# Kernel tuning notes

Measured on AMD Instinct MI355X. Metric: run time of the kernel, lower is better.

The kernel has to match this reference:

```python
import jax, jax.numpy as jnp
import numpy as np

FG_THR = 0.7
BG_THR = 0.3
NUM_PER_IMAGE = 256
NUM_POS_MAX = int(NUM_PER_IMAGE * 0.5)  # positive_ratio = 0.5
BBOX_W = (1.0, 1.0, 1.0, 1.0)
BETA = 1.0 / 9.0


def _permute(t, C):
    # N x (A*C) x H x W -> N x (H*W*A) x C, matching RPNLoss.permute
    N, _, H, W = t.shape
    t = t.reshape(N, -1, C, H, W)
    t = jnp.transpose(t, (0, 3, 4, 1, 2))
    return t.reshape(N, -1, C)


def _iou(a, b):
    # a: [N,4], b: [M,4] -> [N,M] (with +1 box convention, as in source)
    x_tl = jnp.maximum(a[:, None, 0], b[None, :, 0])
    y_tl = jnp.maximum(a[:, None, 1], b[None, :, 1])
    x_rb = jnp.minimum(a[:, None, 2], b[None, :, 2])
    y_rb = jnp.minimum(a[:, None, 3], b[None, :, 3])
    inter = jnp.clip(x_rb - x_tl + 1.0, 0.0) * jnp.clip(y_rb - y_tl + 1.0, 0.0)
    area1 = (a[:, 2] - a[:, 0] + 1.0) * (a[:, 3] - a[:, 1] + 1.0)
    area2 = (b[:, 2] - b[:, 0] + 1.0) * (b[:, 3] - b[:, 1] + 1.0)
    return inter / (area1[:, None] + area2[None, :] - inter)


def _encode(anchors, targets):
    ws = anchors[:, 2] - anchors[:, 0] + 1.0
    hs = anchors[:, 3] - anchors[:, 1] + 1.0
    x_ctr = anchors[:, 0] + 0.5 * ws
    y_ctr = anchors[:, 1] + 0.5 * hs
    t_ws = targets[:, 2] - targets[:, 0] + 1.0
    t_hs = targets[:, 3] - targets[:, 1] + 1.0
    t_x = targets[:, 0] + 0.5 * t_ws
    t_y = targets[:, 1] + 0.5 * t_hs
    wx, wy, ww, wh = BBOX_W
    tx = wx * (t_x - x_ctr) / ws
    ty = wy * (t_y - y_ctr) / hs
    tw = ww * jnp.log(t_ws / ws)
    th = wh * jnp.log(t_hs / hs)
    return jnp.stack([tx, ty, tw, th], axis=1)


def _bce_logits(l, t):
    return jnp.maximum(l, 0.0) - l * t + jnp.log1p(jnp.exp(-jnp.abs(l)))


def _per_image(anchor, logit, breg, size, target, key):
    N = anchor.shape[0]
    ious = _iou(anchor, target)  # [N, M]
    vals = ious.max(axis=1)
    ori = jnp.argmax(ious, axis=1).astype(jnp.int32)
    inds = jnp.where(vals < BG_THR, -1, ori)
    inds = jnp.where((vals >= BG_THR) & (vals < FG_THR), -2, inds)
    # low-quality matches: anchors achieving the per-target max IoU keep their argmax
    col_max = ious.max(axis=0)
    restore = (ious == col_max[None, :]).any(axis=1)
    inds = jnp.where(restore, ori, inds)
    # filter_anchors: keep anchors fully inside the image (size = (h, w))
    inside = (anchor[:, 0] >= 0) & (anchor[:, 1] >= 0) & \
             (anchor[:, 2] <= size[1] - 1.0) & (anchor[:, 3] <= size[0] - 1.0)
    inds = jnp.where(inside, inds, -2)

    pos = inds >= 0
    neg = inds == -1
    # random sampling via random priorities + fixed-size top_k with validity masks
    r = jax.random.uniform(key, (N,))
    pos_vals, pos_idx = jax.lax.top_k(jnp.where(pos, r, -1.0), NUM_POS_MAX)
    valid_pos = pos_vals >= 0.0
    num_pos = valid_pos.sum()
    neg_vals, neg_idx = jax.lax.top_k(jnp.where(neg, r, -1.0), NUM_PER_IMAGE)
    valid_neg = (neg_vals >= 0.0) & (jnp.arange(NUM_PER_IMAGE) < (NUM_PER_IMAGE - num_pos))

    # classification loss terms (BCE with logits); pos target 1, neg target 0
    vp = valid_pos.astype(logit.dtype)
    vn = valid_neg.astype(logit.dtype)
    cls_sum = jnp.sum(_bce_logits(logit[pos_idx], 1.0) * vp) + \
              jnp.sum(_bce_logits(logit[neg_idx], 0.0) * vn)
    count = num_pos + valid_neg.sum()

    m = jnp.clip(inds[pos_idx], 0, None)
    offsets = _encode(anchor[pos_idx], target[m])
    diff = jnp.abs(breg[pos_idx] - offsets)
    sl1 = jnp.where(diff < BETA, 0.5 * diff * diff / BETA, diff - 0.5 * BETA)
    reg_sum = jnp.sum(sl1 * vp[:, None])
    return cls_sum, count, reg_sum


def reference(anchors, logits, bbox_regs, sizes, targets):
    B = anchors.shape[0]
    log = _permute(logits, 1)[..., 0]      # [B, H*W*A]
    breg = _permute(bbox_regs, 4)          # [B, H*W*A, 4]
    keys = jax.random.split(jax.random.key(42), B)
    cls_s, cnt, reg_s = jax.vmap(_per_image)(anchors, log, breg, sizes, targets, keys)
    total = jnp.sum(cnt).astype(anchors.dtype)
    cls_loss = jnp.sum(cls_s) / total
    reg_loss = jnp.sum(reg_s) / total
    return jnp.stack([cls_loss, reg_loss])


def setup_inputs() -> dict:
    key = jax.random.key(0)
    ks = jax.random.split(key, 10)
    B, A, H, W, M = 4, 3, 168, 256, 32
    N = H * W * A
    IMG_H, IMG_W = 800.0, 1333.0
    x1 = jax.random.uniform(ks[0], (B, N)) * 1200.0
    y1 = jax.random.uniform(ks[1], (B, N)) * 700.0
    aw = jax.random.uniform(ks[2], (B, N)) * 300.0 + 16.0
    ah = jax.random.uniform(ks[3], (B, N)) * 300.0 + 16.0
    anchors = jnp.stack([x1, y1, x1 + aw, y1 + ah], axis=-1)  # some out of image -> filtered
    tx1 = jax.random.uniform(ks[4], (B, M)) * 1000.0
    ty1 = jax.random.uniform(ks[5], (B, M)) * 500.0
    tw = jax.random.uniform(ks[6], (B, M)) * 250.0 + 30.0
    th = jax.random.uniform(ks[7], (B, M)) * 200.0 + 30.0
    targets = jnp.stack([tx1, ty1, jnp.minimum(tx1 + tw, IMG_W - 1.0),
                         jnp.minimum(ty1 + th, IMG_H - 1.0)], axis=-1)
    logits = jax.random.normal(ks[8], (B, A, H, W), dtype=jnp.float32)
    bbox_regs = jax.random.normal(ks[9], (B, 4 * A, H, W), dtype=jnp.float32) * 0.1
    sizes = jnp.tile(jnp.array([IMG_H, IMG_W], dtype=jnp.float32), (B, 1))
    return {"anchors": anchors, "logits": logits, "bbox_regs": bbox_regs,
            "sizes": sizes, "targets": targets}
```

## Files before the change

### kernel.cpp

```cpp
#include <hip/hip_runtime.h>
#include <stdint.h>

#define Bn 4
#define An 3
#define Hn 168
#define Wn 256
#define Mn 32
#define HWn (Hn*Wn)
#define Nn (HWn*An)
#define POS_CAP 8192
#define NPERIM 256
#define NPOSMAX 128
#define FG_THR 0.7f
#define BG_THR 0.3f
#define BETA (1.0f/9.0f)

#define NBLK 126
#define APT 4
#define STRIDE (NBLK * 256)
#define BUCKET_CAP 256

#define OFF_POSCNT 0
#define OFF_COUNT  16
#define OFF_CLS    17
#define OFF_REG    18
#define OFF_DONE   19
#define OFF_KEYS   24
#define OFF_PCM    32
#define OFF_WPCM   16160
#define OFF_PLIST  80672
#define OFF_BINCNT 146208
#define OFF_BINBCE 150304
#define OFF_REC    154400
#define OFF_BUCKET 1186592

__device__ __forceinline__ uint32_t rotl32(uint32_t v, int n) { return (v << n) | (v >> (32 - n)); }

__device__ __forceinline__ void tf2x32(uint32_t k0, uint32_t k1, uint32_t x0, uint32_t x1,
                                       uint32_t& o0, uint32_t& o1) {
    uint32_t k2 = k0 ^ k1 ^ 0x1BD11BDAu;
    x0 += k0; x1 += k1;
    x0 += x1; x1 = rotl32(x1, 13); x1 ^= x0;
    x0 += x1; x1 = rotl32(x1, 15); x1 ^= x0;
    x0 += x1; x1 = rotl32(x1, 26); x1 ^= x0;
    x0 += x1; x1 = rotl32(x1, 6);  x1 ^= x0;
    x0 += k1; x1 += k2 + 1u;
    x0 += x1; x1 = rotl32(x1, 17); x1 ^= x0;
    x0 += x1; x1 = rotl32(x1, 29); x1 ^= x0;
    x0 += x1; x1 = rotl32(x1, 16); x1 ^= x0;
    x0 += x1; x1 = rotl32(x1, 24); x1 ^= x0;
    x0 += k2; x1 += k0 + 2u;
    x0 += x1; x1 = rotl32(x1, 13); x1 ^= x0;
    x0 += x1; x1 = rotl32(x1, 15); x1 ^= x0;
    x0 += x1; x1 = rotl32(x1, 26); x1 ^= x0;
    x0 += x1; x1 = rotl32(x1, 6);  x1 ^= x0;
    x0 += k0; x1 += k1 + 3u;
    x0 += x1; x1 = rotl32(x1, 17); x1 ^= x0;
    x0 += x1; x1 = rotl32(x1, 29); x1 ^= x0;
    x0 += x1; x1 = rotl32(x1, 16); x1 ^= x0;
    x0 += x1; x1 = rotl32(x1, 24); x1 ^= x0;
    x0 += k1; x1 += k2 + 4u;
    x0 += x1; x1 = rotl32(x1, 13); x1 ^= x0;
    x0 += x1; x1 = rotl32(x1, 15); x1 ^= x0;
    x0 += x1; x1 = rotl32(x1, 26); x1 ^= x0;
    x0 += x1; x1 = rotl32(x1, 6);  x1 ^= x0;
    x0 += k2; x1 += k0 + 5u;
    o0 = x0; o1 = x1;
}

__device__ __forceinline__ uint32_t rng_m23(uint32_t k0, uint32_t k1, uint32_t i) {
    uint32_t o0, o1;
    tf2x32(k0, k1, 0u, i, o0, o1);
    return (o0 ^ o1) >> 9;
}

__device__ __forceinline__ float iou_one(float a0, float a1, float a2, float a3,
                                         float t0, float t1, float t2, float t3) {
    float xtl = fmaxf(a0, t0), ytl = fmaxf(a1, t1);
    float xrb = fminf(a2, t2), yrb = fminf(a3, t3);
    float iw = fmaxf(xrb - xtl + 1.0f, 0.0f);
    float ih = fmaxf(yrb - ytl + 1.0f, 0.0f);
    float inter = iw * ih;
    float area1 = (a2 - a0 + 1.0f) * (a3 - a1 + 1.0f);
    float area2 = (t2 - t0 + 1.0f) * (t3 - t1 + 1.0f);
    return inter * __builtin_amdgcn_rcpf(area1 + area2 - inter);
}

__device__ __forceinline__ bool sel_less(uint2 a, uint2 b) {
    return (a.x > b.x) || (a.x == b.x && a.y < b.y);
}

__device__ void bitonic_sort_shared(uint2* buf, int n) {
    for (int k = 2; k <= n; k <<= 1) {
        for (int j = k >> 1; j > 0; j >>= 1) {
            for (int t = (int)threadIdx.x; t < n; t += 256) {
                int ixj = t ^ j;
                if (ixj > t) {
                    uint2 x = buf[t], y = buf[ixj];
                    bool up = ((t & k) == 0);
                    bool sw = up ? sel_less(y, x) : sel_less(x, y);
                    if (sw) { buf[t] = y; buf[ixj] = x; }
                }
            }
            __syncthreads();
        }
    }
}

__global__ void __launch_bounds__(256) k1_iou(const float* __restrict__ anchors,
                                              const float* __restrict__ targets,
                                              const float* __restrict__ sizes,
                                              uint32_t* __restrict__ ws) {
    const int b = blockIdx.y, j = blockIdx.x, tid = threadIdx.x;
    const int wid = tid >> 6, lane = tid & 63;

    if (b == 0 && j == 0) {
        if (tid < 24) ws[tid] = 0u;
        for (int q = tid; q < 2 * Bn * 1024; q += 256) ws[OFF_BINCNT + q] = 0u;
        if (tid == 0) {
            for (int bb = 0; bb < Bn; ++bb) {
                uint32_t o0, o1;
                tf2x32(0u, 42u, 0u, (uint32_t)bb, o0, o1);
                ws[OFF_KEYS + 2*bb] = o0; ws[OFF_KEYS + 2*bb + 1] = o1;
            }
        }
    }

    __shared__ float part[4][Mn];
    const int base = j * 256 + tid;
    float4 av[APT];
    #pragma unroll
    for (int k = 0; k < APT; ++k)
        av[k] = ((const float4*)anchors)[b * Nn + base + k * STRIDE];

    float rowmax[APT]; int ori[APT]; uint32_t tie[APT];
    #pragma unroll
    for (int k = 0; k < APT; ++k) { rowmax[k] = -1.0f; ori[k] = 0; tie[k] = 0u; }

    float mycm = 0.0f;
    #pragma unroll 4
    for (int t = 0; t < Mn; ++t) {
        float4 tv = ((const float4*)targets)[b * Mn + t];
        float io[APT];
        float m0 = 0.0f;
        #pragma unroll
        for (int k = 0; k < APT; ++k) {
            io[k] = iou_one(av[k].x, av[k].y, av[k].z, av[k].w, tv.x, tv.y, tv.z, tv.w);
            if (io[k] > rowmax[k]) { rowmax[k] = io[k]; ori[k] = t; }
            m0 = fmaxf(m0, io[k]);
        }
        #pragma unroll
        for (int o = 32; o > 0; o >>= 1) m0 = fmaxf(m0, __shfl_xor(m0, o, 64));
        if (lane == t) mycm = m0;
        #pragma unroll
        for (int k = 0; k < APT; ++k)
            tie[k] |= (io[k] == m0) ? (1u << t) : 0u;
    }

    if (lane < Mn)
        ws[OFF_WPCM + (((size_t)b * NBLK + j) * 4 + wid) * 32 + lane] = __float_as_uint(mycm);
    if (lane < Mn) part[wid][lane] = mycm;
    __syncthreads();
    if (tid < Mn) {
        float v = fmaxf(fmaxf(part[0][tid], part[1][tid]),
                        fmaxf(part[2][tid], part[3][tid]));
        ws[OFF_PCM + ((size_t)b * NBLK + j) * Mn + tid] = __float_as_uint(v);
    }

    const float sh = sizes[b * 2 + 0], sw = sizes[b * 2 + 1];
    #pragma unroll
    for (int k = 0; k < APT; ++k) {
        bool inside = (av[k].x >= 0.0f) && (av[k].y >= 0.0f) &&
                      (av[k].z <= sw - 1.0f) && (av[k].w <= sh - 1.0f);
        uint32_t fl = (uint32_t)ori[k]
                    | (inside ? 32u : 0u)
                    | (rowmax[k] >= FG_THR ? 64u : 0u)
                    | (rowmax[k] < BG_THR ? 128u : 0u);
        ((uint2*)(ws + OFF_REC))[(size_t)b * Nn + base + k * STRIDE] =
            make_uint2(tie[k], fl);
    }
}

__global__ void __launch_bounds__(256) k2_cat(const float* __restrict__ logits,
                                              uint32_t* __restrict__ ws) {
    const int b = blockIdx.y, j = blockIdx.x, tid = threadIdx.x;
    const int wid = tid >> 6, lane = tid & 63;
    __shared__ float cmf[Mn];
    __shared__ float redf[256];

    {
        int t = tid & 31, sub = tid >> 5;
        float acc = 0.0f;
        for (int jj = sub; jj < NBLK; jj += 8)
            acc = fmaxf(acc, __uint_as_float(ws[OFF_PCM + ((size_t)b * NBLK + jj) * Mn + t]));
        redf[tid] = acc;
        __syncthreads();
        if (sub == 0) {
            #pragma unroll
            for (int q = 1; q < 8; ++q) acc = fmaxf(acc, redf[t + 32 * q]);
            cmf[t] = acc;
        }
    }
    __syncthreads();

    uint32_t eqmask;
    {
        bool eq = false;
        if (lane < Mn)
            eq = (ws[OFF_WPCM + (((size_t)b * NBLK + j) * 4 + wid) * 32 + lane]
                  == __float_as_uint(cmf[lane]));
        eqmask = (uint32_t)__ballot(eq);
    }

    const int base = j * 256 + tid;
    const uint32_t key0 = ws[OFF_KEYS + 2 * b], key1 = ws[OFF_KEYS + 2 * b + 1];
    unsigned long long lt_mask = (lane == 63) ? 0x7FFFFFFFFFFFFFFFull
                                              : ((1ull << lane) - 1ull);
    #pragma unroll
    for (int k = 0; k < APT; ++k) {
        const int i = base + k * STRIDE;
        uint2 rec = ((const uint2*)(ws + OFF_REC))[(size_t)b * Nn + i];
        bool restore = (rec.x & eqmask) != 0u;
        uint32_t fl = rec.y;
        uint32_t cat = 0;
        if (fl & 32u) {
            if (restore || (fl & 64u)) cat = 2;
            else if (fl & 128u) cat = 1;
        }
        uint32_t m = rng_m23(key0, key1, (uint32_t)i);
        unsigned long long pmask = __ballot(cat == 2u);
        if (pmask) {
            int leader = __ffsll((long long)pmask) - 1;
            uint32_t bb = 0;
            if (lane == leader) bb = atomicAdd(&ws[OFF_POSCNT + b], (uint32_t)__popcll(pmask));
            bb = __shfl(bb, leader, 64);
            if (cat == 2u) {
                uint32_t p = bb + (uint32_t)__popcll(pmask & lt_mask);
                if (p < POS_CAP)
                    ((uint2*)(ws + OFF_PLIST))[(size_t)b * POS_CAP + p] =
                        make_uint2(m, (uint32_t)i | ((fl & 31u) << 17));
            }
        }
        if (cat == 1u) {
            int bin = (int)(m >> 13);
            uint32_t slot = atomicAdd(&ws[OFF_BINCNT + (b << 10) + bin], 1u);
            if (slot < BUCKET_CAP)
                ((uint2*)(ws + OFF_BUCKET))[((((size_t)b << 10) + bin) << 8) + slot] =
                    make_uint2(m, (uint32_t)i);
            int a = i % An, hw = i / An;
            float l = logits[(b * An + a) * HWn + hw];
            atomicAdd((float*)&ws[OFF_BINBCE + (b << 10) + bin],
                      fmaxf(l, 0.0f) + log1pf(expf(-fabsf(l))));
        }
    }
}

__global__ void __launch_bounds__(256) k3_final(const float* __restrict__ anchors,
                                                const float* __restrict__ targets,
                                                const float* __restrict__ logits,
                                                const float* __restrict__ bregs,
                                                uint32_t* __restrict__ ws,
                                                float* __restrict__ out) {
    const int b = blockIdx.x, tid = threadIdx.x;
    __shared__ union { uint32_t csum[256]; uint2 buf[2048]; } sh;
    __shared__ float red[256];
    __shared__ int s_bd, s_need;
    float cls = 0.0f, reg = 0.0f;

    uint4 hc = ((const uint4*)(ws + OFF_BINCNT + (b << 10)))[tid];
    uint32_t sum = hc.x + hc.y + hc.z + hc.w;
    sh.csum[tid] = sum;
    __syncthreads();
    for (int off = 1; off < 256; off <<= 1) {
        uint32_t mine = sh.csum[tid];
        uint32_t add = (tid + off < 256) ? sh.csum[tid + off] : 0u;
        __syncthreads();
        sh.csum[tid] = mine + add;
        __syncthreads();
    }
    uint32_t pc = ws[OFF_POSCNT + b];
    int num_pos = (pc < (uint32_t)NPOSMAX) ? (int)pc : NPOSMAX;
    int k_neg = NPERIM - num_pos;
    uint32_t total = sh.csum[0];
    if ((int)total < k_neg) {
        if (tid == 0) { s_bd = -1; s_need = 0; }
    } else {
        uint32_t incl = sh.csum[tid];
        uint32_t next = (tid < 255) ? sh.csum[tid + 1] : 0u;
        if ((int)incl >= k_neg && (int)next < k_neg) {
            int cum = (int)next;
            uint32_t hv[4] = { hc.x, hc.y, hc.z, hc.w };
            int boundary = -1, needed = 0;
            #pragma unroll
            for (int q = 3; q >= 0; --q) {
                int c = (int)hv[q];
                if (cum + c >= k_neg) { boundary = 4 * tid + q; needed = k_neg - cum; break; }
                cum += c;
            }
            s_bd = boundary; s_need = needed;
        }
    }
    if (tid == 0) {
        int sel_negs = ((int)total < k_neg) ? (int)total : k_neg;
        atomicAdd(&ws[OFF_COUNT], (uint32_t)(num_pos + sel_negs));
    }
    __syncthreads();
    const int bd = s_bd, need = s_need;

    {
        float4 hb = ((const float4*)(ws + OFF_BINBCE + (b << 10)))[tid];
        int bin0 = 4 * tid;
        if (bin0 + 0 > bd) cls += hb.x;
        if (bin0 + 1 > bd) cls += hb.y;
        if (bin0 + 2 > bd) cls += hb.z;
        if (bin0 + 3 > bd) cls += hb.w;
    }
    __syncthreads();

    if (need > 0) {
        int cnt = (int)ws[OFF_BINCNT + (b << 10) + bd];
        if (cnt > BUCKET_CAP) cnt = BUCKET_CAP;
        const uint2* bkt = (const uint2*)(ws + OFF_BUCKET) + ((((size_t)b << 10) + bd) << 8);
        for (int t = tid; t < cnt; t += 256) sh.buf[t] = bkt[t];
        int npad = 1; while (npad < cnt) npad <<= 1;
        for (int t = tid; t < npad; t += 256) if (t >= cnt) sh.buf[t] = make_uint2(0u, 0xFFFFFFFFu);
        __syncthreads();
        bitonic_sort_shared(sh.buf, npad);
        int sel = (need < cnt) ? need : cnt;
        for (int t = tid; t < sel; t += 256) {
            int i = (int)sh.buf[t].y;
            int a = i % An, hw = i / An;
            float l = logits[(b * An + a) * HWn + hw];
            cls += fmaxf(l, 0.0f) + log1pf(expf(-fabsf(l)));
        }
    }
    __syncthreads();

    {
        int pci = (pc < (uint32_t)POS_CAP) ? (int)pc : POS_CAP;
        const uint2* plist = (const uint2*)(ws + OFF_PLIST) + (size_t)b * POS_CAP;
        int psel = (pci < NPOSMAX) ? pci : NPOSMAX;
        bool use_buf = false;
        if (pci > NPOSMAX) {
            int n = (pci < 2048) ? pci : 2048;
            for (int t = tid; t < n; t += 256) sh.buf[t] = plist[t];
            int npad = 1; while (npad < n) npad <<= 1;
            for (int t = tid; t < npad; t += 256) if (t >= n) sh.buf[t] = make_uint2(0u, 0xFFFFFFFFu);
            __syncthreads();
            bitonic_sort_shared(sh.buf, npad);
            use_buf = true;
            psel = (NPOSMAX < n) ? NPOSMAX : n;
        }
        for (int t = tid; t < psel; t += 256) {
            uint32_t packed = use_buf ? sh.buf[t].y : plist[t].y;
            int i = (int)(packed & 0x1FFFFu);
            int orit = (int)(packed >> 17);
            int a = i % An, hw = i / An;
            float l = logits[(b * An + a) * HWn + hw];
            cls += fmaxf(l, 0.0f) - l + log1pf(expf(-fabsf(l)));
            float4 avx = ((const float4*)anchors)[b * Nn + i];
            float4 tv = ((const float4*)targets)[b * Mn + orit];
            float aws = avx.z - avx.x + 1.0f, ahs = avx.w - avx.y + 1.0f;
            float axc = avx.x + 0.5f * aws, ayc = avx.y + 0.5f * ahs;
            float tws = tv.z - tv.x + 1.0f, ths = tv.w - tv.y + 1.0f;
            float txc = tv.x + 0.5f * tws, tyc = tv.y + 0.5f * ths;
            float off0 = (txc - axc) / aws;
            float off1 = (tyc - ayc) / ahs;
            float off2 = logf(tws / aws);
            float off3 = logf(ths / ahs);
            float br0 = bregs[(b * 12 + a * 4 + 0) * HWn + hw];
            float br1 = bregs[(b * 12 + a * 4 + 1) * HWn + hw];
            float br2 = bregs[(b * 12 + a * 4 + 2) * HWn + hw];
            float br3 = bregs[(b * 12 + a * 4 + 3) * HWn + hw];
            float d;
            d = fabsf(br0 - off0); reg += (d < BETA) ? 0.5f * d * d / BETA : d - 0.5f * BETA;
            d = fabsf(br1 - off1); reg += (d < BETA) ? 0.5f * d * d / BETA : d - 0.5f * BETA;
            d = fabsf(br2 - off2); reg += (d < BETA) ? 0.5f * d * d / BETA : d - 0.5f * BETA;
            d = fabsf(br3 - off3); reg += (d < BETA) ? 0.5f * d * d / BETA : d - 0.5f * BETA;
        }
    }

    red[tid] = cls;
    __syncthreads();
    for (int s = 128; s > 0; s >>= 1) {
        if (tid < s) red[tid] += red[tid + s];
        __syncthreads();
    }
    if (tid == 0 && red[0] != 0.0f) atomicAdd((float*)&ws[OFF_CLS], red[0]);
    __syncthreads();
    red[tid] = reg;
    __syncthreads();
    for (int s = 128; s > 0; s >>= 1) {
        if (tid < s) red[tid] += red[tid + s];
        __syncthreads();
    }
    if (tid == 0) {
        if (red[0] != 0.0f) atomicAdd((float*)&ws[OFF_REG], red[0]);
        __threadfence();
        uint32_t old = atomicAdd(&ws[OFF_DONE], 1u);
        if (old == Bn - 1) {
            float cls_tot = __uint_as_float(atomicAdd(&ws[OFF_CLS], 0u));
            float reg_tot = __uint_as_float(atomicAdd(&ws[OFF_REG], 0u));
            float cnt = (float)atomicAdd(&ws[OFF_COUNT], 0u);
            out[0] = cls_tot / cnt;
            out[1] = reg_tot / cnt;
        }
    }
}

extern "C" void kernel_launch(void* const* d_in, const int* in_sizes, int n_in,
                              void* d_out, int out_size, void* d_ws, size_t ws_size,
                              hipStream_t stream) {
    const float* anchors = (const float*)d_in[0];
    const float* logits  = (const float*)d_in[1];
    const float* bregs   = (const float*)d_in[2];
    const float* sizes   = (const float*)d_in[3];
    const float* targets = (const float*)d_in[4];
    float* out = (float*)d_out;
    uint32_t* ws = (uint32_t*)d_ws;

    k1_iou<<<dim3(NBLK, Bn), dim3(256), 0, stream>>>(anchors, targets, sizes, ws);
    k2_cat<<<dim3(NBLK, Bn), dim3(256), 0, stream>>>(logits, ws);
    k3_final<<<dim3(Bn), dim3(256), 0, stream>>>(anchors, targets, logits, bregs, ws, out);
}
```

Before: 158.1 us.

## Fuse categorization into IoU kernel and defer tie-restore anchors to final kernel

Removes the separate k2_cat pass and its per-anchor record buffer. k1 now classifies anchors directly: clear positives and negatives are emitted at once, and only anchors with a tie bit that might be restored go to a compacted list. k3 computes the per-target column max, builds per-wave equality masks and resolves that deferred list. Workspace zeroing moves into a small init kernel. This saves a full read and write of per-anchor records and a launch, but puts more serial work, atomics and a possibly long tie list into the 4-block final kernel.

```diff
diff --git a/kernel.cpp b/kernel.cpp
--- a/kernel.cpp
+++ b/kernel.cpp
@@ -9,6 +9,7 @@
 #define HWn (Hn*Wn)
 #define Nn (HWn*An)
 #define POS_CAP 8192
+#define TIE_CAP 49152
 #define NPERIM 256
 #define NPOSMAX 128
 #define FG_THR 0.7f
@@ -18,21 +19,22 @@
 #define NBLK 126
 #define APT 4
 #define STRIDE (NBLK * 256)
+#define NWAVES (NBLK * 4)
 #define BUCKET_CAP 256
 
 #define OFF_POSCNT 0
-#define OFF_COUNT  16
-#define OFF_CLS    17
-#define OFF_REG    18
-#define OFF_DONE   19
-#define OFF_KEYS   24
-#define OFF_PCM    32
-#define OFF_WPCM   16160
-#define OFF_PLIST  80672
-#define OFF_BINCNT 146208
-#define OFF_BINBCE 150304
-#define OFF_REC    154400
-#define OFF_BUCKET 1186592
+#define OFF_TIECNT 4
+#define OFF_COUNT  8
+#define OFF_CLS    9
+#define OFF_REG    10
+#define OFF_DONE   11
+#define OFF_BINCNT 16
+#define OFF_BINBCE 4112
+#define ZERO_WORDS 8208
+#define OFF_WPCM   8208
+#define OFF_PLIST  72720
+#define OFF_BUCKET 138256
+#define OFF_TIE    2235408
 
 __device__ __forceinline__ uint32_t rotl32(uint32_t v, int n) { return (v << n) | (v >> (32 - n)); }
 
@@ -74,6 +76,10 @@
     return (o0 ^ o1) >> 9;
 }
 
+__device__ __forceinline__ uint32_t vload(const uint32_t* p) {
+    return *(const volatile uint32_t*)p;
+}
+
 __device__ __forceinline__ float iou_one(float a0, float a1, float a2, float a3,
                                          float t0, float t1, float t2, float t3) {
     float xtl = fmaxf(a0, t0), ytl = fmaxf(a1, t1);
@@ -84,6 +90,10 @@
     float area1 = (a2 - a0 + 1.0f) * (a3 - a1 + 1.0f);
     float area2 = (t2 - t0 + 1.0f) * (t3 - t1 + 1.0f);
     return inter * __builtin_amdgcn_rcpf(area1 + area2 - inter);
+}
+
+__device__ __forceinline__ float bce0(float l) {
+    return fmaxf(l, 0.0f) + log1pf(expf(-fabsf(l)));
 }
 
 __device__ __forceinline__ bool sel_less(uint2 a, uint2 b) {
@@ -107,26 +117,22 @@
     }
 }
 
+__global__ void __launch_bounds__(256) k0_init(uint32_t* __restrict__ ws) {
+    int i = blockIdx.x * 256 + (int)threadIdx.x;
+    if (i < ZERO_WORDS) ws[i] = 0u;
+}
+
 __global__ void __launch_bounds__(256) k1_iou(const float* __restrict__ anchors,
                                               const float* __restrict__ targets,
                                               const float* __restrict__ sizes,
+                                              const float* __restrict__ logits,
                                               uint32_t* __restrict__ ws) {
     const int b = blockIdx.y, j = blockIdx.x, tid = threadIdx.x;
     const int wid = tid >> 6, lane = tid & 63;
 
-    if (b == 0 && j == 0) {
-        if (tid < 24) ws[tid] = 0u;
-        for (int q = tid; q < 2 * Bn * 1024; q += 256) ws[OFF_BINCNT + q] = 0u;
-        if (tid == 0) {
-            for (int bb = 0; bb < Bn; ++bb) {
-                uint32_t o0, o1;
-                tf2x32(0u, 42u, 0u, (uint32_t)bb, o0, o1);
-                ws[OFF_KEYS + 2*bb] = o0; ws[OFF_KEYS + 2*bb + 1] = o1;
-            }
-        }
-    }
-
-    __shared__ float part[4][Mn];
+    uint32_t key0, key1;
+    tf2x32(0u, 42u, 0u, (uint32_t)b, key0, key1);
+
     const int base = j * 256 + tid;
     float4 av[APT];
     #pragma unroll
@@ -158,90 +164,52 @@
     }
 
     if (lane < Mn)
-        ws[OFF_WPCM + (((size_t)b * NBLK + j) * 4 + wid) * 32 + lane] = __float_as_uint(mycm);
-    if (lane < Mn) part[wid][lane] = mycm;
-    __syncthreads();
-    if (tid < Mn) {
-        float v = fmaxf(fmaxf(part[0][tid], part[1][tid]),
-                        fmaxf(part[2][tid], part[3][tid]));
-        ws[OFF_PCM + ((size_t)b * NBLK + j) * Mn + tid] = __float_as_uint(v);
-    }
+        ws[OFF_WPCM + ((size_t)b * NWAVES + (j * 4 + wid)) * 32 + lane] = __float_as_uint(mycm);
 
     const float sh = sizes[b * 2 + 0], sw = sizes[b * 2 + 1];
-    #pragma unroll
-    for (int k = 0; k < APT; ++k) {
-        bool inside = (av[k].x >= 0.0f) && (av[k].y >= 0.0f) &&
-                      (av[k].z <= sw - 1.0f) && (av[k].w <= sh - 1.0f);
-        uint32_t fl = (uint32_t)ori[k]
-                    | (inside ? 32u : 0u)
-                    | (rowmax[k] >= FG_THR ? 64u : 0u)
-                    | (rowmax[k] < BG_THR ? 128u : 0u);
-        ((uint2*)(ws + OFF_REC))[(size_t)b * Nn + base + k * STRIDE] =
-            make_uint2(tie[k], fl);
-    }
-}
-
-__global__ void __launch_bounds__(256) k2_cat(const float* __restrict__ logits,
-                                              uint32_t* __restrict__ ws) {
-    const int b = blockIdx.y, j = blockIdx.x, tid = threadIdx.x;
-    const int wid = tid >> 6, lane = tid & 63;
-    __shared__ float cmf[Mn];
-    __shared__ float redf[256];
-
-    {
-        int t = tid & 31, sub = tid >> 5;
-        float acc = 0.0f;
-        for (int jj = sub; jj < NBLK; jj += 8)
-            acc = fmaxf(acc, __uint_as_float(ws[OFF_PCM + ((size_t)b * NBLK + jj) * Mn + t]));
-        redf[tid] = acc;
-        __syncthreads();
-        if (sub == 0) {
-            #pragma unroll
-            for (int q = 1; q < 8; ++q) acc = fmaxf(acc, redf[t + 32 * q]);
-            cmf[t] = acc;
-        }
-    }
-    __syncthreads();
-
-    uint32_t eqmask;
-    {
-        bool eq = false;
-        if (lane < Mn)
-            eq = (ws[OFF_WPCM + (((size_t)b * NBLK + j) * 4 + wid) * 32 + lane]
-                  == __float_as_uint(cmf[lane]));
-        eqmask = (uint32_t)__ballot(eq);
-    }
-
-    const int base = j * 256 + tid;
-    const uint32_t key0 = ws[OFF_KEYS + 2 * b], key1 = ws[OFF_KEYS + 2 * b + 1];
     unsigned long long lt_mask = (lane == 63) ? 0x7FFFFFFFFFFFFFFFull
                                               : ((1ull << lane) - 1ull);
     #pragma unroll
     for (int k = 0; k < APT; ++k) {
         const int i = base + k * STRIDE;
-        uint2 rec = ((const uint2*)(ws + OFF_REC))[(size_t)b * Nn + i];
-        bool restore = (rec.x & eqmask) != 0u;
-        uint32_t fl = rec.y;
-        uint32_t cat = 0;
-        if (fl & 32u) {
-            if (restore || (fl & 64u)) cat = 2;
-            else if (fl & 128u) cat = 1;
-        }
+        bool inside = (av[k].x >= 0.0f) && (av[k].y >= 0.0f) &&
+                      (av[k].z <= sw - 1.0f) && (av[k].w <= sh - 1.0f);
+        bool fg = rowmax[k] >= FG_THR;
+        bool bg = rowmax[k] < BG_THR;
+        bool posn  = inside && fg;
+        bool defern = inside && !fg && (tie[k] != 0u);
+        bool negn  = inside && bg && (tie[k] == 0u);
         uint32_t m = rng_m23(key0, key1, (uint32_t)i);
-        unsigned long long pmask = __ballot(cat == 2u);
+
+        unsigned long long pmask = __ballot(posn);
         if (pmask) {
             int leader = __ffsll((long long)pmask) - 1;
             uint32_t bb = 0;
             if (lane == leader) bb = atomicAdd(&ws[OFF_POSCNT + b], (uint32_t)__popcll(pmask));
             bb = __shfl(bb, leader, 64);
-            if (cat == 2u) {
+            if (posn) {
                 uint32_t p = bb + (uint32_t)__popcll(pmask & lt_mask);
                 if (p < POS_CAP)
                     ((uint2*)(ws + OFF_PLIST))[(size_t)b * POS_CAP + p] =
-                        make_uint2(m, (uint32_t)i | ((fl & 31u) << 17));
+                        make_uint2(m, (uint32_t)i | ((uint32_t)ori[k] << 17));
             }
         }
-        if (cat == 1u) {
+        unsigned long long dmask = __ballot(defern);
+        if (dmask) {
+            int leader = __ffsll((long long)dmask) - 1;
+            uint32_t bb = 0;
+            if (lane == leader) bb = atomicAdd(&ws[OFF_TIECNT + b], (uint32_t)__popcll(dmask));
+            bb = __shfl(bb, leader, 64);
+            if (defern) {
+                uint32_t p = bb + (uint32_t)__popcll(dmask & lt_mask);
+                if (p < TIE_CAP)
+                    ((uint4*)(ws + OFF_TIE))[(size_t)b * TIE_CAP + p] =
+                        make_uint4(tie[k], m,
+                                   (uint32_t)i | ((uint32_t)ori[k] << 17) | (bg ? (1u << 22) : 0u),
+                                   0u);
+            }
+        }
+        if (negn) {
             int bin = (int)(m >> 13);
             uint32_t slot = atomicAdd(&ws[OFF_BINCNT + (b << 10) + bin], 1u);
             if (slot < BUCKET_CAP)
@@ -249,8 +217,7 @@
                     make_uint2(m, (uint32_t)i);
             int a = i % An, hw = i / An;
             float l = logits[(b * An + a) * HWn + hw];
-            atomicAdd((float*)&ws[OFF_BINBCE + (b << 10) + bin],
-                      fmaxf(l, 0.0f) + log1pf(expf(-fabsf(l))));
+            atomicAdd((float*)&ws[OFF_BINBCE + (b << 10) + bin], bce0(l));
         }
     }
 }
@@ -262,13 +229,73 @@
                                                 uint32_t* __restrict__ ws,
                                                 float* __restrict__ out) {
     const int b = blockIdx.x, tid = threadIdx.x;
+    __shared__ uint32_t cmbits[Mn];
+    __shared__ float redf[256];
+    __shared__ uint32_t eq[512];
+    __shared__ float lbce[1024];
     __shared__ union { uint32_t csum[256]; uint2 buf[2048]; } sh;
     __shared__ float red[256];
     __shared__ int s_bd, s_need;
     float cls = 0.0f, reg = 0.0f;
 
-    uint4 hc = ((const uint4*)(ws + OFF_BINCNT + (b << 10)))[tid];
-    uint32_t sum = hc.x + hc.y + hc.z + hc.w;
+    {
+        int t = tid & 31, sub = tid >> 5;
+        float acc = 0.0f;
+        for (int w = sub; w < NWAVES; w += 8)
+            acc = fmaxf(acc, __uint_as_float(ws[OFF_WPCM + ((size_t)b * NWAVES + w) * 32 + t]));
+        redf[tid] = acc;
+        __syncthreads();
+        if (sub == 0) {
+            #pragma unroll
+            for (int q = 1; q < 8; ++q) acc = fmaxf(acc, redf[t + 32 * q]);
+            cmbits[t] = __float_as_uint(acc);
+        }
+    }
+    for (int q = tid; q < 1024; q += 256) lbce[q] = 0.0f;
+    __syncthreads();
+
+    for (int w = tid; w < NWAVES; w += 256) {
+        const uint32_t* wp = ws + OFF_WPCM + ((size_t)b * NWAVES + w) * 32;
+        uint32_t e = 0;
+        #pragma unroll 8
+        for (int t2 = 0; t2 < Mn; ++t2)
+            e |= (wp[t2] == cmbits[t2]) ? (1u << t2) : 0u;
+        eq[w] = e;
+    }
+    __syncthreads();
+
+    {
+        uint32_t tcu = vload(ws + OFF_TIECNT + b);
+        int tcnt = (tcu < (uint32_t)TIE_CAP) ? (int)tcu : TIE_CAP;
+        const uint4* tlist = (const uint4*)(ws + OFF_TIE) + (size_t)b * TIE_CAP;
+        for (int idx = tid; idx < tcnt; idx += 256) {
+            uint4 e = tlist[idx];
+            int i = (int)(e.z & 0x1FFFFu);
+            int w = (i % STRIDE) >> 6;
+            if (e.x & eq[w]) {
+                uint32_t p = atomicAdd(&ws[OFF_POSCNT + b], 1u);
+                if (p < POS_CAP)
+                    ((uint2*)(ws + OFF_PLIST))[(size_t)b * POS_CAP + p] =
+                        make_uint2(e.y, e.z & 0x3FFFFFu);
+            } else if (e.z & (1u << 22)) {
+                uint32_t m = e.y;
+                int bin = (int)(m >> 13);
+                uint32_t slot = atomicAdd(&ws[OFF_BINCNT + (b << 10) + bin], 1u);
+                if (slot < BUCKET_CAP)
+                    ((uint2*)(ws + OFF_BUCKET))[((((size_t)b << 10) + bin) << 8) + slot] =
+                        make_uint2(m, (uint32_t)i);
+                int a = i % An, hw = i / An;
+                float l = logits[(b * An + a) * HWn + hw];
+                atomicAdd(&lbce[bin], bce0(l));
+            }
+        }
+    }
+    __syncthreads();
+
+    uint32_t c4[4];
+    #pragma unroll
+    for (int q = 0; q < 4; ++q) c4[q] = vload(ws + OFF_BINCNT + (b << 10) + 4 * tid + q);
+    uint32_t sum = c4[0] + c4[1] + c4[2] + c4[3];
     sh.csum[tid] = sum;
     __syncthreads();
     for (int off = 1; off < 256; off <<= 1) {
@@ -278,7 +305,7 @@
         sh.csum[tid] = mine + add;
         __syncthreads();
     }
-    uint32_t pc = ws[OFF_POSCNT + b];
+    uint32_t pc = vload(ws + OFF_POSCNT + b);
     int num_pos = (pc < (uint32_t)NPOSMAX) ? (int)pc : NPOSMAX;
     int k_neg = NPERIM - num_pos;
     uint32_t total = sh.csum[0];
@@ -289,11 +316,10 @@
         uint32_t next = (tid < 255) ? sh.csum[tid + 1] : 0u;
         if ((int)incl >= k_neg && (int)next < k_neg) {
             int cum = (int)next;
-            uint32_t hv[4] = { hc.x, hc.y, hc.z, hc.w };
             int boundary = -1, needed = 0;
             #pragma unroll
             for (int q = 3; q >= 0; --q) {
-                int c = (int)hv[q];
+                int c = (int)c4[q];
                 if (cum + c >= k_neg) { boundary = 4 * tid + q; needed = k_neg - cum; break; }
                 cum += c;
             }
@@ -307,18 +333,18 @@
     __syncthreads();
     const int bd = s_bd, need = s_need;
 
-    {
-        float4 hb = ((const float4*)(ws + OFF_BINBCE + (b << 10)))[tid];
-        int bin0 = 4 * tid;
-        if (bin0 + 0 > bd) cls += hb.x;
-        if (bin0 + 1 > bd) cls += hb.y;
-        if (bin0 + 2 > bd) cls += hb.z;
-        if (bin0 + 3 > bd) cls += hb.w;
+    #pragma unroll
+    for (int q = 0; q < 4; ++q) {
+        int bin = 4 * tid + q;
+        if (bin > bd) {
+            float gb = __uint_as_float(vload(ws + OFF_BINBCE + (b << 10) + bin));
+            cls += gb + lbce[bin];
+        }
     }
     __syncthreads();
 
     if (need > 0) {
-        int cnt = (int)ws[OFF_BINCNT + (b << 10) + bd];
+        int cnt = (int)vload(ws + OFF_BINCNT + (b << 10) + bd);
         if (cnt > BUCKET_CAP) cnt = BUCKET_CAP;
         const uint2* bkt = (const uint2*)(ws + OFF_BUCKET) + ((((size_t)b << 10) + bd) << 8);
         for (int t = tid; t < cnt; t += 256) sh.buf[t] = bkt[t];
@@ -331,7 +357,7 @@
             int i = (int)sh.buf[t].y;
             int a = i % An, hw = i / An;
             float l = logits[(b * An + a) * HWn + hw];
-            cls += fmaxf(l, 0.0f) + log1pf(expf(-fabsf(l)));
+            cls += bce0(l);
         }
     }
     __syncthreads();
@@ -419,7 +445,7 @@
     float* out = (float*)d_out;
     uint32_t* ws = (uint32_t*)d_ws;
 
-    k1_iou<<<dim3(NBLK, Bn), dim3(256), 0, stream>>>(anchors, targets, sizes, ws);
-    k2_cat<<<dim3(NBLK, Bn), dim3(256), 0, stream>>>(logits, ws);
+    k0_init<<<dim3((ZERO_WORDS + 255) / 256), dim3(256), 0, stream>>>(ws);
+    k1_iou<<<dim3(NBLK, Bn), dim3(256), 0, stream>>>(anchors, targets, sizes, logits, ws);
     k3_final<<<dim3(Bn), dim3(256), 0, stream>>>(anchors, targets, logits, bregs, ws, out);
 }
```

Result: slower. 310.7 us (+96.5%).
